# Kernel optimization log

Measured on AMD Instinct MI355X. Metric: run time of the kernel, lower is better.

Reference implementation:

```python
import jax, jax.numpy as jnp
import numpy as np

B, SE, HE, DE = 32, 256, 512, 2
HD = DE * HE            # decoder hidden (h0 reshape implies Hd = De*He)
ED = 256                # label embedding dim
N = 8192                # seq label num (output_size)
T = 20                  # decode_max_seq_len (eval path)
KE = VE = 1024
MD = 256
EIN = ED + HE           # LSTM input size
EOS_ID = 0
SPARCE_RATE = 0.8
NEG = -1.0e7
MAXV = 1.0e9
EPS = 1e-8


def setup_inputs() -> dict:
    key = jax.random.key(0)
    ks = jax.random.split(key, 20)
    s = 0.05
    return {
        'encoded_hidden_embeddings': jax.random.normal(ks[0], (B, SE, HE), jnp.float32),
        'hidden': jax.random.normal(ks[1], (DE, B, HE), jnp.float32),
        'cell': jax.random.normal(ks[2], (DE, B, HE), jnp.float32),
        'text_lengths': jax.random.randint(ks[3], (B,), 1, SE + 1),
        'encoder_mask': jnp.ones((B, SE), bool),
        'memory_key_mask': jnp.ones((B, KE), bool),
        'memory_key_embedding': jax.random.normal(ks[4], (B, KE, MD), jnp.float32),
        'memory_value_mask': jnp.ones((B, VE), bool),
        'memory_value_embedding': jax.random.normal(ks[5], (B, VE, MD), jnp.float32),
        # parameters
        'W_ih': jax.random.normal(ks[6], (4 * HD, EIN), jnp.float32) * s,
        'W_hh': jax.random.normal(ks[7], (4 * HD, HD), jnp.float32) * s,
        'b_ih': jnp.zeros((4 * HD,), jnp.float32),
        'b_hh': jnp.zeros((4 * HD,), jnp.float32),
        'mlp_W1': jax.random.normal(ks[8], (HD, HD), jnp.float32) * s,
        'mlp_b1': jnp.zeros((HD,), jnp.float32),
        'mlp_W2': jax.random.normal(ks[9], (N, HD), jnp.float32) * s,
        'mlp_b2': jnp.zeros((N,), jnp.float32),
        'emb_table': jax.random.normal(ks[10], (N, ED), jnp.float32) * s,
        'dense_W': jax.random.normal(ks[11], (HE, ED), jnp.float32) * s,
        'dense_b': jnp.zeros((HE,), jnp.float32),
        'read_W': jax.random.normal(ks[12], (MD, EIN), jnp.float32) * s,
        'read_b': jnp.zeros((MD,), jnp.float32),
    }


def _cos(a, b):
    num = jnp.sum(a * b, axis=-1)
    den = jnp.maximum(jnp.linalg.norm(a, axis=-1) * jnp.linalg.norm(b, axis=-1), EPS)
    return num / den


def _lstm(x, h, c, W_ih, W_hh, b_ih, b_hh):
    g = x @ W_ih.T + b_ih + h @ W_hh.T + b_hh
    i, f, gg, o = jnp.split(g, 4, axis=-1)  # torch gate order i,f,g,o
    c1 = jax.nn.sigmoid(f) * c + jax.nn.sigmoid(i) * jnp.tanh(gg)
    h1 = jax.nn.sigmoid(o) * jnp.tanh(c1)
    return h1, c1


def _forward(enc, hidden, cell, encoder_mask, memory_key_mask, memory_value_mask,
             mem_k, mem_v, W_ih, W_hh, b_ih, b_hh, mlp_W1, mlp_b1, mlp_W2, mlp_b2,
             emb_table, dense_W, dense_b, read_W, read_b):
    h0 = jnp.transpose(hidden, (1, 0, 2)).reshape(B, HD)
    c0 = jnp.transpose(cell, (1, 0, 2)).reshape(B, HD)
    pad = jnp.where(encoder_mask, 0.0, -MAXV).astype(enc.dtype)  # (B,Se)
    sent = enc[:, 0, :]                                           # (B,He)
    x0 = jnp.zeros((B, EIN), enc.dtype)
    mask0 = jnp.zeros((B, N), enc.dtype)

    def step(carry, _):
        h, c, x, lmask = carry
        h, c = _lstm(x, h, c, W_ih, W_hh, b_ih, b_hh)
        hid = jax.nn.relu(h @ mlp_W1.T + mlp_b1)
        logits = hid @ mlp_W2.T + mlp_b2 + lmask          # (B,N)
        nid = jnp.argmax(logits, axis=-1)                 # (B,) greedy decode
        lab = emb_table[nid]                              # (B,Ed)
        lmask = lmask.at[jnp.arange(B), nid].set(NEG)     # scatter-mask used ids
        lmask = lmask.at[:, EOS_ID].set(0.0)              # EOS always allowed
        q = lab @ dense_W.T + dense_b                     # (B,He)
        score = jnp.einsum('bse,be->bs', enc, q) + pad
        w = jax.nn.softmax(score, axis=-1)
        attn = jnp.einsum('bse,bs->be', enc, w)
        x = jnp.concatenate([lab, sent + attn], axis=-1)  # (B,Ed+He)
        mq = x @ read_W.T + read_b                        # (B,Md)
        ksim = _cos(mq[:, None, :], mem_k)                # (B,Ke)
        return (h, c, x, lmask), (logits, nid, ksim)

    _, (outputs, next_ids, key_sims) = jax.lax.scan(step, (h0, c0, x0, mask0), None, length=T)
    outputs = jnp.transpose(outputs, (1, 0, 2))           # (B,T,N)
    next_ids = next_ids.T                                 # (B,T)
    key_sims = jnp.transpose(key_sims, (1, 0, 2))         # (B,T,Ke)

    key_sim = jnp.max(key_sims, axis=1)                   # (B,Ke)
    key_sim = jnp.where(key_sim < 0, 0.0, key_sim)
    # mapping_weight: pairwise cosine between memory keys and values (B,Ke,Ve)
    mw = _cos(mem_k[:, :, None, :], mem_v[:, None, :, :])
    keep = (mw >= jnp.max(mw, axis=-1, keepdims=True)) & (mw >= SPARCE_RATE)
    mw = jnp.where(keep, mw, 0.0)
    val_sim = jnp.einsum('bk,bkv->bv', key_sim, mw)       # (B,Ve)
    key_out = jnp.where(memory_key_mask, key_sim, -1.0)
    val_out = jnp.where(memory_value_mask, val_sim, -1.0)
    return outputs, next_ids, key_out, val_out


def reference(encoded_hidden_embeddings, hidden, cell, text_lengths, encoder_mask,
              memory_key_mask, memory_key_embedding, memory_value_mask, memory_value_embedding,
              W_ih, W_hh, b_ih, b_hh, mlp_W1, mlp_b1, mlp_W2, mlp_b2,
              emb_table, dense_W, dense_b, read_W, read_b):
    del text_lengths  # unused in module math
    return _forward(encoded_hidden_embeddings, hidden, cell, encoder_mask,
                    memory_key_mask, memory_value_mask, memory_key_embedding,
                    memory_value_embedding, W_ih, W_hh, b_ih, b_hh,
                    mlp_W1, mlp_b1, mlp_W2, mlp_b2, emb_table,
                    dense_W, dense_b, read_W, read_b)
```

## Files before the change

kernel.cpp:

```cpp
#include <hip/hip_runtime.h>
#include <cstdint>
#include <cstddef>

#define B_   32
#define SE_  256
#define HE_  512
#define HD_  1024
#define ED_  256
#define N_   8192
#define T_   20
#define KE_  1024
#define VE_  1024
#define MD_  256
#define EIN_ 768
#define NEG_   (-10000000.0f)
#define MAXV_  (1000000000.0f)
#define EPS_   (1e-8f)
#define SPARSE_ 0.8f
#define GATE_  0.78f

#define NLOGB (N_/16)

#define O_IDS  (B_*T_*N_)
#define O_KEY  (O_IDS + B_*T_)
#define O_VAL  (O_KEY + B_*KE_)

typedef __attribute__((ext_vector_type(8))) short short8;
typedef __attribute__((ext_vector_type(4))) float floatx4;

__device__ __forceinline__ float sigf(float v) { return 1.0f / (1.0f + expf(-v)); }

__device__ __forceinline__ short f2bf(float f) {
    union { float f; unsigned u; } v; v.f = f;
    unsigned r = v.u + 0x7FFFu + ((v.u >> 16) & 1u);
    return (short)(r >> 16);
}
__device__ __forceinline__ short8 pack8(const float4 a, const float4 b) {
    short8 r;
    r[0]=f2bf(a.x); r[1]=f2bf(a.y); r[2]=f2bf(a.z); r[3]=f2bf(a.w);
    r[4]=f2bf(b.x); r[5]=f2bf(b.y); r[6]=f2bf(b.z); r[7]=f2bf(b.w);
    return r;
}

__device__ __forceinline__ bool mask_is_b8(const void* p) {
    unsigned u = *(const unsigned*)p;
    return u > 0xFFu;
}
__device__ __forceinline__ bool mask_at(const void* p, int idx, bool b8) {
    return b8 ? (((const unsigned char*)p)[idx] != 0)
              : (((const int*)p)[idx] != 0);
}

__global__ __launch_bounds__(256) void k_init(
    const float* __restrict__ hidden, const float* __restrict__ cell,
    const float* __restrict__ enc, const void* __restrict__ encmask,
    float* __restrict__ h, float* __restrict__ c, float* __restrict__ x,
    float* __restrict__ lmask, float* __restrict__ sent, float* __restrict__ pad,
    float* __restrict__ key_run, float* __restrict__ val_sim, float* __restrict__ rowmax)
{
    int idx = blockIdx.x * 256 + threadIdx.x;
    lmask[idx] = 0.0f;
    if (idx < B_ * HD_) {
        int b = idx >> 10, j = idx & 1023;
        int d = j >> 9, e = j & 511;
        h[idx] = hidden[((size_t)d * B_ + b) * HE_ + e];
        c[idx] = cell  [((size_t)d * B_ + b) * HE_ + e];
        key_run[idx] = -1e30f;
        val_sim[idx] = 0.0f;
        rowmax[idx] = 0.0f;
    }
    if (idx < B_ * EIN_) x[idx] = 0.0f;
    if (idx < B_ * HE_) {
        int b = idx >> 9, e = idx & 511;
        sent[idx] = enc[(size_t)b * SE_ * HE_ + e];
    }
    if (idx < B_ * SE_) {
        bool b8 = mask_is_b8(encmask);
        pad[idx] = mask_at(encmask, idx, b8) ? 0.0f : -MAXV_;
    }
}

__global__ __launch_bounds__(256) void k_norms(
    const float* __restrict__ mem_k, const float* __restrict__ mem_v,
    float* __restrict__ normk, float* __restrict__ normv)
{
    int lane = threadIdx.x & 63;
    int wave = (blockIdx.x * 256 + threadIdx.x) >> 6;
    for (int row = wave; row < 2 * B_ * KE_; row += 1024) {
        const float* base = (row < B_ * KE_) ? (mem_k + (size_t)row * MD_)
                                             : (mem_v + (size_t)(row - B_ * KE_) * MD_);
        float4 v = ((const float4*)base)[lane];
        float s = v.x*v.x + v.y*v.y + v.z*v.z + v.w*v.w;
        for (int m = 32; m; m >>= 1) s += __shfl_xor(s, m, 64);
        if (lane == 0) {
            if (row < B_ * KE_) normk[row] = sqrtf(s);
            else                normv[row - B_ * KE_] = sqrtf(s);
        }
    }
}

__global__ __launch_bounds__(256) void k_rowmax_mfma(
    const float* __restrict__ mem_k, const float* __restrict__ mem_v,
    const float* __restrict__ normk, const float* __restrict__ normv,
    float* __restrict__ rowmax)
{
    __shared__ __align__(16) short Vs[64 * 256];
    const int tid = threadIdx.x, lane = tid & 63, w = tid >> 6;
    const int kt = blockIdx.x, vseg = blockIdx.y, b = blockIdx.z;
    const int rowbase = kt * 128 + w * 32;
    const int lrow = lane & 15, lq = lane >> 4;

    float nk[2][4];
    #pragma unroll
    for (int rg = 0; rg < 2; ++rg)
        #pragma unroll
        for (int reg = 0; reg < 4; ++reg)
            nk[rg][reg] = normk[b * KE_ + rowbase + rg * 16 + lq * 4 + reg];

    short8 af[2][8];
    #pragma unroll
    for (int rg = 0; rg < 2; ++rg) {
        const float* arow = mem_k + ((size_t)(b * KE_ + rowbase + rg * 16 + lrow)) * MD_;
        #pragma unroll
        for (int kc = 0; kc < 8; ++kc) {
            const float* p = arow + kc * 32 + lq * 8;
            float4 f0 = *(const float4*)p;
            float4 f1 = *(const float4*)(p + 4);
            af[rg][kc] = pack8(f0, f1);
        }
    }

    float rmax[2][4];
    #pragma unroll
    for (int rg = 0; rg < 2; ++rg)
        #pragma unroll
        for (int reg = 0; reg < 4; ++reg) rmax[rg][reg] = -1e30f;

    for (int vs = vseg * 4; vs < vseg * 4 + 4; ++vs) {
        __syncthreads();
        #pragma unroll
        for (int i = 0; i < 8; ++i) {
            int lin = tid + i * 256;
            int r = lin >> 5, cg = lin & 31;
            const float* p = mem_v + ((size_t)(b * VE_ + vs * 64 + r)) * MD_ + cg * 8;
            float4 f0 = *(const float4*)p;
            float4 f1 = *(const float4*)(p + 4);
            int byt = (r * 512 + cg * 16) ^ ((r & 7) << 4);
            *(short8*)((char*)Vs + byt) = pack8(f0, f1);
        }
        __syncthreads();

        for (int vsub = 0; vsub < 4; ++vsub) {
            int vrow = vsub * 16 + lrow;
            float nv = normv[b * VE_ + vs * 64 + vrow];
            short8 bfr[8];
            #pragma unroll
            for (int kc = 0; kc < 8; ++kc) {
                int byt = (vrow * 512 + kc * 64 + lq * 16) ^ ((vrow & 7) << 4);
                bfr[kc] = *(const short8*)((char*)Vs + byt);
            }
            #pragma unroll
            for (int rg = 0; rg < 2; ++rg) {
                floatx4 acc = {0.0f, 0.0f, 0.0f, 0.0f};
                #pragma unroll
                for (int kc = 0; kc < 8; ++kc)
                    acc = __builtin_amdgcn_mfma_f32_16x16x32_bf16(af[rg][kc], bfr[kc], acc, 0, 0, 0);
                #pragma unroll
                for (int reg = 0; reg < 4; ++reg) {
                    float cs = acc[reg] / fmaxf(nk[rg][reg] * nv, EPS_);
                    rmax[rg][reg] = fmaxf(rmax[rg][reg], cs);
                }
            }
        }
    }
    #pragma unroll
    for (int rg = 0; rg < 2; ++rg)
        #pragma unroll
        for (int reg = 0; reg < 4; ++reg) {
            float v = rmax[rg][reg];
            v = fmaxf(v, __shfl_xor(v, 1, 64));
            v = fmaxf(v, __shfl_xor(v, 2, 64));
            v = fmaxf(v, __shfl_xor(v, 4, 64));
            v = fmaxf(v, __shfl_xor(v, 8, 64));
            if (lrow == 0) {
                int* p = (int*)&rowmax[(size_t)b * KE_ + rowbase + rg * 16 + lq * 4 + reg];
                atomicMax(p, __float_as_int(fmaxf(v, 0.0f)));
            }
        }
}

__device__ __forceinline__ float wave_dot(const float* __restrict__ row, const float* vl, int quads)
{
    int lane = threadIdx.x & 63;
    float s = 0.0f;
    for (int q = lane; q < quads; q += 64) {
        float4 a = ((const float4*)row)[q];
        float4 x = ((const float4*)vl)[q];
        s = fmaf(a.x, x.x, s); s = fmaf(a.y, x.y, s);
        s = fmaf(a.z, x.z, s); s = fmaf(a.w, x.w, s);
    }
    for (int m = 32; m; m >>= 1) s += __shfl_xor(s, m, 64);
    return s;
}

__global__ __launch_bounds__(256) void k_gates2(
    const float* __restrict__ x, const float* __restrict__ W_ih,
    const float* __restrict__ h_in, const float* __restrict__ W_hh,
    const float* __restrict__ b_ih, const float* __restrict__ b_hh,
    float* __restrict__ c_st, float* __restrict__ h_out)
{
    __shared__ __align__(16) float Xs[32 * 256];
    __shared__ float red[8][32][17];
    const int tid = threadIdx.x;
    const int kg = tid & 15, jg = (tid >> 4) & 3, bg = tid >> 6;
    const int ch0 = blockIdx.x * 2;

    float acc[2][8];
    #pragma unroll
    for (int jv = 0; jv < 2; ++jv)
        #pragma unroll
        for (int bv = 0; bv < 8; ++bv) acc[jv][bv] = 0.0f;

    for (int k0 = 0; k0 < EIN_ + HD_; k0 += 256) {
        const bool second = (k0 >= EIN_);
        const float* Xsrc = second ? h_in : x;
        const float* Wsrc = second ? W_hh : W_ih;
        const int srcK = second ? HD_ : EIN_;
        const int ks = second ? (k0 - EIN_) : k0;
        __syncthreads();
        #pragma unroll
        for (int i = 0; i < 8; ++i) {
            int lin = tid + i * 256;
            int bb = lin >> 6, q = lin & 63;
            *(float4*)&Xs[bb * 256 + q * 4] = *(const float4*)(Xsrc + (size_t)bb * srcK + ks + q * 4);
        }
        __syncthreads();
        #pragma unroll
        for (int qq = 0; qq < 4; ++qq) {
            const int qc = kg + qq * 16;
            float4 wv[2];
            #pragma unroll
            for (int jv = 0; jv < 2; ++jv) {
                int row = jg * HD_ + ch0 + jv;
                wv[jv] = *(const float4*)(Wsrc + (size_t)row * srcK + ks + qc * 4);
            }
            #pragma unroll
            for (int bv = 0; bv < 8; ++bv) {
                float4 x4 = *(const float4*)&Xs[(bg * 8 + bv) * 256 + qc * 4];
                #pragma unroll
                for (int jv = 0; jv < 2; ++jv) {
                    acc[jv][bv] = fmaf(wv[jv].x, x4.x, acc[jv][bv]);
                    acc[jv][bv] = fmaf(wv[jv].y, x4.y, acc[jv][bv]);
                    acc[jv][bv] = fmaf(wv[jv].z, x4.z, acc[jv][bv]);
                    acc[jv][bv] = fmaf(wv[jv].w, x4.w, acc[jv][bv]);
                }
            }
        }
    }
    #pragma unroll
    for (int jv = 0; jv < 2; ++jv)
        #pragma unroll
        for (int bv = 0; bv < 8; ++bv)
            red[jg * 2 + jv][bg * 8 + bv][kg] = acc[jv][bv];
    __syncthreads();
    if (tid < 64) {
        const int c2 = tid >> 5, b = tid & 31;
        float g4[4];
        #pragma unroll
        for (int gate = 0; gate < 4; ++gate) {
            float s = 0.0f;
            #pragma unroll
            for (int k = 0; k < 16; ++k) s += red[gate * 2 + c2][b][k];
            int row = gate * HD_ + ch0 + c2;
            g4[gate] = s + b_ih[row] + b_hh[row];
        }
        int idx = b * HD_ + ch0 + c2;
        float c1 = sigf(g4[1]) * c_st[idx] + sigf(g4[0]) * tanhf(g4[2]);
        h_out[idx] = sigf(g4[3]) * tanhf(c1);
        c_st[idx] = c1;
    }
}

__global__ __launch_bounds__(256) void k_mlp1(
    const float* __restrict__ X, const float* __restrict__ W,
    const float* __restrict__ bias, float* __restrict__ out)
{
    __shared__ __align__(16) float Xs[32 * 256];
    __shared__ float red[4][32][17];
    const int tid = threadIdx.x;
    const int kg = tid & 15, jg = (tid >> 4) & 3, bg = tid >> 6;
    const int jbase = blockIdx.x * 4;

    float acc[8];
    #pragma unroll
    for (int bv = 0; bv < 8; ++bv) acc[bv] = 0.0f;

    for (int k0 = 0; k0 < HD_; k0 += 256) {
        __syncthreads();
        #pragma unroll
        for (int i = 0; i < 8; ++i) {
            int lin = tid + i * 256;
            int bb = lin >> 6, q = lin & 63;
            *(float4*)&Xs[bb * 256 + q * 4] = *(const float4*)(X + (size_t)bb * HD_ + k0 + q * 4);
        }
        __syncthreads();
        #pragma unroll
        for (int qq = 0; qq < 4; ++qq) {
            const int qc = kg + qq * 16;
            float4 w4 = *(const float4*)(W + (size_t)(jbase + jg) * HD_ + k0 + qc * 4);
            #pragma unroll
            for (int bv = 0; bv < 8; ++bv) {
                float4 x4 = *(const float4*)&Xs[(bg * 8 + bv) * 256 + qc * 4];
                acc[bv] = fmaf(w4.x, x4.x, acc[bv]);
                acc[bv] = fmaf(w4.y, x4.y, acc[bv]);
                acc[bv] = fmaf(w4.z, x4.z, acc[bv]);
                acc[bv] = fmaf(w4.w, x4.w, acc[bv]);
            }
        }
    }
    #pragma unroll
    for (int bv = 0; bv < 8; ++bv)
        red[jg][bg * 8 + bv][kg] = acc[bv];
    __syncthreads();
    if (tid < 128) {
        int jjo = tid >> 5, b = tid & 31;
        float s = 0.0f;
        #pragma unroll
        for (int k = 0; k < 16; ++k) s += red[jjo][b][k];
        int jo = jbase + jjo;
        out[(size_t)b * HD_ + jo] = fmaxf(s + bias[jo], 0.0f);
    }
}

__global__ __launch_bounds__(256) void k_logits(
    const float* __restrict__ hid, const float* __restrict__ W2,
    const float* __restrict__ b2, const float* __restrict__ lmask,
    float* __restrict__ lg_out, float* __restrict__ pval, int* __restrict__ pidx)
{
    __shared__ __align__(16) float Xs[32 * 256];
    __shared__ float red[16][32][17];
    const int tid = threadIdx.x;
    const int kg = tid & 15, jg = (tid >> 4) & 3, bg = tid >> 6;
    const int jbase = blockIdx.x * 16;

    float acc[4][8];
    #pragma unroll
    for (int jv = 0; jv < 4; ++jv)
        #pragma unroll
        for (int bv = 0; bv < 8; ++bv) acc[jv][bv] = 0.0f;

    for (int k0 = 0; k0 < HD_; k0 += 256) {
        __syncthreads();
        #pragma unroll
        for (int i = 0; i < 8; ++i) {
            int lin = tid + i * 256;
            int bb = lin >> 6, q = lin & 63;
            *(float4*)&Xs[bb * 256 + q * 4] = *(const float4*)(hid + (size_t)bb * HD_ + k0 + q * 4);
        }
        __syncthreads();
        #pragma unroll
        for (int qq = 0; qq < 4; ++qq) {
            const int qc = kg + qq * 16;
            float4 wv[4];
            #pragma unroll
            for (int jv = 0; jv < 4; ++jv)
                wv[jv] = *(const float4*)(W2 + (size_t)(jbase + jg * 4 + jv) * HD_ + k0 + qc * 4);
            #pragma unroll
            for (int bv = 0; bv < 8; ++bv) {
                float4 x4 = *(const float4*)&Xs[(bg * 8 + bv) * 256 + qc * 4];
                #pragma unroll
                for (int jv = 0; jv < 4; ++jv) {
                    acc[jv][bv] = fmaf(wv[jv].x, x4.x, acc[jv][bv]);
                    acc[jv][bv] = fmaf(wv[jv].y, x4.y, acc[jv][bv]);
                    acc[jv][bv] = fmaf(wv[jv].z, x4.z, acc[jv][bv]);
                    acc[jv][bv] = fmaf(wv[jv].w, x4.w, acc[jv][bv]);
                }
            }
        }
    }
    #pragma unroll
    for (int jv = 0; jv < 4; ++jv)
        #pragma unroll
        for (int bv = 0; bv < 8; ++bv)
            red[jg * 4 + jv][bg * 8 + bv][kg] = acc[jv][bv];
    __syncthreads();
    for (int o = tid; o < 16 * B_; o += 256) {
        int jjo = o >> 5, b = o & 31;
        float s = 0.0f;
        #pragma unroll
        for (int k = 0; k < 16; ++k) s += red[jjo][b][k];
        int jo = jbase + jjo;
        s += b2[jo] + lmask[(size_t)b * N_ + jo];
        lg_out[(size_t)b * (T_ * N_) + jo] = s;
        red[jjo][b][16] = s;
    }
    __syncthreads();
    if (tid < 32) {
        int b = tid;
        float best = -1e38f; int bi = 0;
        #pragma unroll
        for (int jjo = 0; jjo < 16; ++jjo) {
            float v = red[jjo][b][16];
            if (v > best) { best = v; bi = jjo; }
        }
        pval[(size_t)b * NLOGB + blockIdx.x] = best;
        pidx[(size_t)b * NLOGB + blockIdx.x] = jbase + bi;
    }
}

__global__ __launch_bounds__(256) void k_merge(
    const float* __restrict__ pval, const int* __restrict__ pidx,
    float* __restrict__ d_out, int t, int* __restrict__ nidbuf,
    float* __restrict__ lmask, const float* __restrict__ emb,
    const float* __restrict__ dense_W, const float* __restrict__ dense_b,
    float* __restrict__ qbuf)
{
    __shared__ float sv[256];
    __shared__ int   si[256];
    __shared__ __align__(16) float lab[ED_];
    const int b = blockIdx.x, tid = threadIdx.x;
    float best = -1e38f; int bi = N_;
    for (int p = tid; p < NLOGB; p += 256) {
        float v = pval[(size_t)b * NLOGB + p];
        int   i = pidx[(size_t)b * NLOGB + p];
        if (v > best || (v == best && i < bi)) { best = v; bi = i; }
    }
    sv[tid] = best; si[tid] = bi;
    __syncthreads();
    for (int s = 128; s > 0; s >>= 1) {
        if (tid < s) {
            float v2 = sv[tid + s]; int i2 = si[tid + s];
            if (v2 > sv[tid] || (v2 == sv[tid] && i2 < si[tid])) { sv[tid] = v2; si[tid] = i2; }
        }
        __syncthreads();
    }
    int nid = si[0];
    if (tid == 0) {
        nidbuf[b] = nid;
        d_out[O_IDS + (size_t)b * T_ + t] = (float)nid;
        lmask[(size_t)b * N_ + nid] = NEG_;
        lmask[(size_t)b * N_] = 0.0f;
    }
    lab[tid] = emb[(size_t)nid * ED_ + tid];
    __syncthreads();
    const float4* Lq = (const float4*)lab;
    #pragma unroll
    for (int jj = 0; jj < 2; ++jj) {
        int j = tid + jj * 256;
        const float4* Wq = (const float4*)(dense_W + (size_t)j * ED_);
        float s0 = 0.0f, s1 = 0.0f, s2 = 0.0f, s3 = 0.0f;
        #pragma unroll
        for (int q = 0; q < 64; q += 4) {
            float4 w0 = Wq[q],   x0 = Lq[q];
            float4 w1 = Wq[q+1], x1 = Lq[q+1];
            float4 w2 = Wq[q+2], x2 = Lq[q+2];
            float4 w3 = Wq[q+3], x3 = Lq[q+3];
            s0 = fmaf(w0.x,x0.x,s0); s0 = fmaf(w0.y,x0.y,s0); s0 = fmaf(w0.z,x0.z,s0); s0 = fmaf(w0.w,x0.w,s0);
            s1 = fmaf(w1.x,x1.x,s1); s1 = fmaf(w1.y,x1.y,s1); s1 = fmaf(w1.z,x1.z,s1); s1 = fmaf(w1.w,x1.w,s1);
            s2 = fmaf(w2.x,x2.x,s2); s2 = fmaf(w2.y,x2.y,s2); s2 = fmaf(w2.z,x2.z,s2); s2 = fmaf(w2.w,x2.w,s2);
            s3 = fmaf(w3.x,x3.x,s3); s3 = fmaf(w3.y,x3.y,s3); s3 = fmaf(w3.z,x3.z,s3); s3 = fmaf(w3.w,x3.w,s3);
        }
        qbuf[(size_t)b * HE_ + j] = dense_b[j] + ((s0 + s1) + (s2 + s3));
    }
}

__global__ __launch_bounds__(256) void k_attn1(
    const float* __restrict__ qg, const float* __restrict__ enc,
    const float* __restrict__ pad, float* __restrict__ part)
{
    __shared__ __align__(16) float ql[HE_];
    __shared__ float sc_l[32];
    __shared__ float wp_l[32];
    const int b = blockIdx.y, sc = blockIdx.x;
    const int tid = threadIdx.x, lane = tid & 63, w = tid >> 6;
    ql[tid] = qg[(size_t)b * HE_ + tid];
    ql[tid + 256] = qg[(size_t)b * HE_ + tid + 256];
    __syncthreads();

    #pragma unroll
    for (int i = 0; i < 8; ++i) {
        int sl = w + i * 4;
        int s = sc * 32 + sl;
        float v = wave_dot(enc + ((size_t)b * SE_ + s) * HE_, ql, HE_ / 4);
        if (lane == 0) sc_l[sl] = v + pad[b * SE_ + s];
    }
    __syncthreads();

    float m = -1e38f;
    #pragma unroll
    for (int i = 0; i < 32; ++i) m = fmaxf(m, sc_l[i]);
    if (tid < 32) wp_l[tid] = expf(sc_l[tid] - m);
    __syncthreads();
    float esum = 0.0f;
    #pragma unroll
    for (int i = 0; i < 32; ++i) esum += wp_l[i];

    float a0 = 0.0f, a1 = 0.0f;
    for (int i = 0; i < 32; ++i) {
        float wv = wp_l[i];
        const float* er = enc + ((size_t)b * SE_ + sc * 32 + i) * HE_;
        a0 = fmaf(wv, er[tid], a0);
        a1 = fmaf(wv, er[tid + 256], a1);
    }
    float* pb = part + ((size_t)b * 8 + sc) * 516;
    pb[tid] = a0;
    pb[256 + tid] = a1;
    if (tid == 0) { pb[512] = m; pb[513] = esum; }
}

__global__ __launch_bounds__(256) void k_attn2read(
    const float* __restrict__ part, const float* __restrict__ sent,
    const int* __restrict__ nidbuf, const float* __restrict__ emb,
    const float* __restrict__ read_W, const float* __restrict__ read_b,
    float* __restrict__ xg, float* __restrict__ mqg)
{
    __shared__ float ms[8], es[8];
    __shared__ __align__(16) float xl[EIN_];
    const int qv = blockIdx.x, b = blockIdx.y;
    const int tid = threadIdx.x;
    if (tid < 8) {
        ms[tid] = part[((size_t)b * 8 + tid) * 516 + 512];
        es[tid] = part[((size_t)b * 8 + tid) * 516 + 513];
    }
    __syncthreads();
    float m = -1e38f;
    #pragma unroll
    for (int c = 0; c < 8; ++c) m = fmaxf(m, ms[c]);
    float scale[8];
    float denom = 0.0f;
    #pragma unroll
    for (int c = 0; c < 8; ++c) { scale[c] = expf(ms[c] - m); denom += es[c] * scale[c]; }
    float inv = 1.0f / denom;
    float a0 = 0.0f, a1 = 0.0f;
    #pragma unroll
    for (int c = 0; c < 8; ++c) {
        const float* pb = part + ((size_t)b * 8 + c) * 516;
        a0 = fmaf(scale[c], pb[tid], a0);
        a1 = fmaf(scale[c], pb[256 + tid], a1);
    }
    a0 *= inv; a1 *= inv;
    int nid = nidbuf[b];
    xl[tid]             = emb[(size_t)nid * ED_ + tid];
    xl[ED_ + tid]       = sent[(size_t)b * HE_ + tid]       + a0;
    xl[ED_ + 256 + tid] = sent[(size_t)b * HE_ + 256 + tid] + a1;
    __syncthreads();
    if (qv == 0) {
        float* xr = xg + (size_t)b * EIN_;
        xr[tid] = xl[tid]; xr[tid + 256] = xl[tid + 256]; xr[tid + 512] = xl[tid + 512];
    }
    const int r = qv * 64 + (tid >> 2), kq = tid & 3;
    const float4* Wq = (const float4*)(read_W + (size_t)r * EIN_ + kq * 192);
    const float4* xq = (const float4*)(xl + kq * 192);
    float s0 = 0.0f, s1 = 0.0f, s2 = 0.0f, s3 = 0.0f;
    #pragma unroll
    for (int q = 0; q < 48; q += 4) {
        float4 w0 = Wq[q],   v0 = xq[q];
        float4 w1 = Wq[q+1], v1 = xq[q+1];
        float4 w2 = Wq[q+2], v2 = xq[q+2];
        float4 w3 = Wq[q+3], v3 = xq[q+3];
        s0 = fmaf(w0.x,v0.x,s0); s0 = fmaf(w0.y,v0.y,s0); s0 = fmaf(w0.z,v0.z,s0); s0 = fmaf(w0.w,v0.w,s0);
        s1 = fmaf(w1.x,v1.x,s1); s1 = fmaf(w1.y,v1.y,s1); s1 = fmaf(w1.z,v1.z,s1); s1 = fmaf(w1.w,v1.w,s1);
        s2 = fmaf(w2.x,v2.x,s2); s2 = fmaf(w2.y,v2.y,s2); s2 = fmaf(w2.z,v2.z,s2); s2 = fmaf(w2.w,v2.w,s2);
        s3 = fmaf(w3.x,v3.x,s3); s3 = fmaf(w3.y,v3.y,s3); s3 = fmaf(w3.z,v3.z,s3); s3 = fmaf(w3.w,v3.w,s3);
    }
    float s = ((s0 + s1) + (s2 + s3));
    s += __shfl_xor(s, 1, 64);
    s += __shfl_xor(s, 2, 64);
    if (kq == 0) mqg[(size_t)b * MD_ + r] = s + read_b[r];
}

__global__ __launch_bounds__(256) void k_ksim(
    const float* __restrict__ mqg,
    const float* __restrict__ mem_k, const float* __restrict__ normk,
    float* __restrict__ key_run)
{
    __shared__ __align__(16) float mql[MD_];
    __shared__ float red[256];
    const int b = blockIdx.y, kt = blockIdx.x;
    const int tid = threadIdx.x, lane = tid & 63, w = tid >> 6;
    float mv = mqg[(size_t)b * MD_ + tid];
    mql[tid] = mv;
    red[tid] = mv * mv;
    __syncthreads();
    for (int s = 128; s > 0; s >>= 1) { if (tid < s) red[tid] += red[tid + s]; __syncthreads(); }
    float nmq = sqrtf(red[0]);

    int base = kt * 64 + w * 16;
    for (int i = 0; i < 16; ++i) {
        int k = base + i;
        float num = wave_dot(mem_k + ((size_t)b * KE_ + k) * MD_, mql, MD_ / 4);
        if (lane == 0) {
            float cs = num / fmaxf(nmq * normk[b * KE_ + k], EPS_);
            float o = key_run[b * KE_ + k];
            key_run[b * KE_ + k] = fmaxf(o, cs);
        }
    }
}

__global__ __launch_bounds__(256) void k_keyfinal(
    float* __restrict__ key_run, const void* __restrict__ kmask, float* __restrict__ d_out)
{
    int idx = blockIdx.x * 256 + threadIdx.x;
    bool b8 = mask_is_b8(kmask);
    float v = key_run[idx];
    v = (v < 0.0f) ? 0.0f : v;
    key_run[idx] = v;
    d_out[O_KEY + idx] = mask_at(kmask, idx, b8) ? v : -1.0f;
}

__global__ __launch_bounds__(256) void k_val(
    const float* __restrict__ rowmax, const float* __restrict__ mem_k, const float* __restrict__ mem_v,
    const float* __restrict__ normk, const float* __restrict__ normv,
    const float* __restrict__ key_sim, float* __restrict__ val_sim)
{
    int idx = blockIdx.x * 256 + threadIdx.x;
    if (rowmax[idx] < GATE_) return;
    int b = idx >> 10;
    const float* krow = mem_k + (size_t)idx * MD_;
    float nk = normk[idx];
    float ks = key_sim[idx];
    float rm = -1e30f;
    for (int v = 0; v < VE_; ++v) {
        const float* vrow = mem_v + ((size_t)b * VE_ + v) * MD_;
        float d = 0.0f;
        for (int e = 0; e < MD_; ++e) d = fmaf(krow[e], vrow[e], d);
        float cs = d / fmaxf(nk * normv[b * VE_ + v], EPS_);
        rm = fmaxf(rm, cs);
    }
    float thr = fmaxf(rm, SPARSE_);
    for (int v = 0; v < VE_; ++v) {
        const float* vrow = mem_v + ((size_t)b * VE_ + v) * MD_;
        float d = 0.0f;
        for (int e = 0; e < MD_; ++e) d = fmaf(krow[e], vrow[e], d);
        float cs = d / fmaxf(nk * normv[b * VE_ + v], EPS_);
        if (cs >= thr) atomicAdd(&val_sim[(size_t)b * VE_ + v], ks * cs);
    }
}

__global__ __launch_bounds__(256) void k_valout(
    const float* __restrict__ val_sim, const void* __restrict__ vmask, float* __restrict__ d_out)
{
    int idx = blockIdx.x * 256 + threadIdx.x;
    bool b8 = mask_is_b8(vmask);
    d_out[O_VAL + idx] = mask_at(vmask, idx, b8) ? val_sim[idx] : -1.0f;
}

extern "C" void kernel_launch(void* const* d_in, const int* in_sizes, int n_in,
                              void* d_out_v, int out_size, void* d_ws, size_t ws_size,
                              hipStream_t stream)
{
    const float* enc      = (const float*)d_in[0];
    const float* hidden   = (const float*)d_in[1];
    const float* cell     = (const float*)d_in[2];
    const void*  encmask  = d_in[4];
    const void*  kmask    = d_in[5];
    const float* mem_k    = (const float*)d_in[6];
    const void*  vmask    = d_in[7];
    const float* mem_v    = (const float*)d_in[8];
    const float* W_ih     = (const float*)d_in[9];
    const float* W_hh     = (const float*)d_in[10];
    const float* b_ih     = (const float*)d_in[11];
    const float* b_hh     = (const float*)d_in[12];
    const float* mlp_W1   = (const float*)d_in[13];
    const float* mlp_b1   = (const float*)d_in[14];
    const float* mlp_W2   = (const float*)d_in[15];
    const float* mlp_b2   = (const float*)d_in[16];
    const float* emb      = (const float*)d_in[17];
    const float* dense_W  = (const float*)d_in[18];
    const float* dense_b  = (const float*)d_in[19];
    const float* read_W   = (const float*)d_in[20];
    const float* read_b   = (const float*)d_in[21];
    float* d_out = (float*)d_out_v;
    float* ws = (float*)d_ws;

    float* hA      = ws;
    float* hB      = ws + 32768;
    float* c       = ws + 65536;
    float* x       = ws + 98304;
    float* hid     = ws + 122880;
    float* lmask   = ws + 155648;
    float* sent    = ws + 417792;
    float* pad     = ws + 434176;
    float* key_run = ws + 442368;
    float* val_sim = ws + 475136;
    float* normk   = ws + 507904;
    float* normv   = ws + 540672;
    float* rowmax  = ws + 573440;
    int*   nidbuf  = (int*)(ws + 606208);
    float* mqg     = ws + 606272;
    float* qbuf    = ws + 614464;
    float* part    = ws + 630848;
    float* pval    = ws + 762944;
    int*   pidx    = (int*)(ws + 779328);

    k_init<<<1024, 256, 0, stream>>>(hidden, cell, enc, encmask, hA, c, x, lmask, sent, pad, key_run, val_sim, rowmax);
    k_norms<<<256, 256, 0, stream>>>(mem_k, mem_v, normk, normv);
    k_rowmax_mfma<<<dim3(8, 4, 32), 256, 0, stream>>>(mem_k, mem_v, normk, normv, rowmax);

    const float* hin = hA;
    float* hout = hB;
    for (int t = 0; t < T_; ++t) {
        k_gates2<<<512, 256, 0, stream>>>(x, W_ih, hin, W_hh, b_ih, b_hh, c, hout);
        k_mlp1<<<HD_ / 4, 256, 0, stream>>>(hout, mlp_W1, mlp_b1, hid);
        k_logits<<<N_ / 16, 256, 0, stream>>>(hid, mlp_W2, mlp_b2, lmask,
                                              d_out + (size_t)t * N_, pval, pidx);
        k_merge<<<B_, 256, 0, stream>>>(pval, pidx, d_out, t, nidbuf, lmask,
                                        emb, dense_W, dense_b, qbuf);
        k_attn1<<<dim3(8, B_), 256, 0, stream>>>(qbuf, enc, pad, part);
        k_attn2read<<<dim3(4, B_), 256, 0, stream>>>(part, sent, nidbuf, emb, read_W, read_b, x, mqg);
        k_ksim<<<dim3(16, B_), 256, 0, stream>>>(mqg, mem_k, normk, key_run);
        float* tmp = (float*)hin; hin = hout; hout = tmp;
    }

    k_keyfinal<<<128, 256, 0, stream>>>(key_run, kmask, d_out);
    k_val<<<128, 256, 0, stream>>>(rowmax, mem_k, mem_v, normk, normv, key_run, val_sim);
    k_valout<<<128, 256, 0, stream>>>(val_sim, vmask, d_out);
}
```

Measured before the change: 2.796 ms.

## Fuse key-similarity into next step's gates kernel to overlap independent work

```diff
diff --git a/kernel.cpp b/kernel.cpp
--- a/kernel.cpp
+++ b/kernel.cpp
@@ -203,15 +203,44 @@
     return s;
 }
 
-__global__ __launch_bounds__(256) void k_gates2(
+__global__ __launch_bounds__(256) void k_gates_ksim(
     const float* __restrict__ x, const float* __restrict__ W_ih,
     const float* __restrict__ h_in, const float* __restrict__ W_hh,
     const float* __restrict__ b_ih, const float* __restrict__ b_hh,
-    float* __restrict__ c_st, float* __restrict__ h_out)
+    float* __restrict__ c_st, float* __restrict__ h_out,
+    const float* __restrict__ mqg, const float* __restrict__ mem_k,
+    const float* __restrict__ normk, float* __restrict__ key_run, int do_ksim)
 {
     __shared__ __align__(16) float Xs[32 * 256];
     __shared__ float red[8][32][17];
     const int tid = threadIdx.x;
+
+    if (blockIdx.x >= 512) {
+        if (!do_ksim) return;
+        float* mql  = Xs;
+        float* red2 = Xs + 256;
+        const int u = blockIdx.x - 512;
+        const int kt = u & 15, b = u >> 4;
+        const int lane = tid & 63, w = tid >> 6;
+        float mv = mqg[(size_t)b * MD_ + tid];
+        mql[tid] = mv;
+        red2[tid] = mv * mv;
+        __syncthreads();
+        for (int s = 128; s > 0; s >>= 1) { if (tid < s) red2[tid] += red2[tid + s]; __syncthreads(); }
+        float nmq = sqrtf(red2[0]);
+        int base = kt * 64 + w * 16;
+        for (int i = 0; i < 16; ++i) {
+            int k = base + i;
+            float num = wave_dot(mem_k + ((size_t)b * KE_ + k) * MD_, mql, MD_ / 4);
+            if (lane == 0) {
+                float cs = num / fmaxf(nmq * normk[b * KE_ + k], EPS_);
+                float o = key_run[b * KE_ + k];
+                key_run[b * KE_ + k] = fmaxf(o, cs);
+            }
+        }
+        return;
+    }
+
     const int kg = tid & 15, jg = (tid >> 4) & 3, bg = tid >> 6;
     const int ch0 = blockIdx.x * 2;
 
@@ -561,7 +590,7 @@
         s0 = fmaf(w0.x,v0.x,s0); s0 = fmaf(w0.y,v0.y,s0); s0 = fmaf(w0.z,v0.z,s0); s0 = fmaf(w0.w,v0.w,s0);
         s1 = fmaf(w1.x,v1.x,s1); s1 = fmaf(w1.y,v1.y,s1); s1 = fmaf(w1.z,v1.z,s1); s1 = fmaf(w1.w,v1.w,s1);
         s2 = fmaf(w2.x,v2.x,s2); s2 = fmaf(w2.y,v2.y,s2); s2 = fmaf(w2.z,v2.z,s2); s2 = fmaf(w2.w,v2.w,s2);
-        s3 = fmaf(w3.x,v3.x,s3); s3 = fmaf(w3.y,v3.y,s3); s3 = fmaf(w3.z,v3.z,s3); s3 = fmaf(w3.w,v3.w,s3);
+        s3 = fmaf(w3.x,v3.x,s3); s3 = fmaf(w3.z,v3.z,s3); s3 = fmaf(w3.y,v3.y,s3); s3 = fmaf(w3.w,v3.w,s3);
     }
     float s = ((s0 + s1) + (s2 + s3));
     s += __shfl_xor(s, 1, 64);
@@ -700,7 +729,8 @@
     const float* hin = hA;
     float* hout = hB;
     for (int t = 0; t < T_; ++t) {
-        k_gates2<<<512, 256, 0, stream>>>(x, W_ih, hin, W_hh, b_ih, b_hh, c, hout);
+        k_gates_ksim<<<1024, 256, 0, stream>>>(x, W_ih, hin, W_hh, b_ih, b_hh, c, hout,
+                                               mqg, mem_k, normk, key_run, t > 0 ? 1 : 0);
         k_mlp1<<<HD_ / 4, 256, 0, stream>>>(hout, mlp_W1, mlp_b1, hid);
         k_logits<<<N_ / 16, 256, 0, stream>>>(hid, mlp_W2, mlp_b2, lmask,
                                               d_out + (size_t)t * N_, pval, pidx);
@@ -708,9 +738,9 @@
                                         emb, dense_W, dense_b, qbuf);
         k_attn1<<<dim3(8, B_), 256, 0, stream>>>(qbuf, enc, pad, part);
         k_attn2read<<<dim3(4, B_), 256, 0, stream>>>(part, sent, nidbuf, emb, read_W, read_b, x, mqg);
-        k_ksim<<<dim3(16, B_), 256, 0, stream>>>(mqg, mem_k, normk, key_run);
         float* tmp = (float*)hin; hin = hout; hout = tmp;
     }
+    k_ksim<<<dim3(16, B_), 256, 0, stream>>>(mqg, mem_k, normk, key_run);
 
     k_keyfinal<<<128, 256, 0, stream>>>(key_run, kmask, d_out);
     k_val<<<128, 256, 0, stream>>>(rowmax, mem_k, mem_v, normk, normv, key_run, val_sim);
```

Measured after the change: 2.552 ms. 1.1x faster.
